# Performance work log

Measured on AMD Instinct MI355X. Metric: run time of the kernel, lower is better.

Reference implementation:

```python
import jax, jax.numpy as jnp
import numpy as np

N_ITERS = 2
N_NODES = 50000
N_EDGES = 400000
NODE_DIM = 128
EDGE_DIM = 128
MLP_HIDDEN = 128


def _gru_cell(x, h, W_ih, W_hh, b_ih, b_hh):
    # torch.nn.GRUCell math. W_ih: [3H, in], W_hh: [3H, H]
    gi = x @ W_ih.T + b_ih
    gh = h @ W_hh.T + b_hh
    i_r, i_z, i_n = jnp.split(gi, 3, axis=-1)
    h_r, h_z, h_n = jnp.split(gh, 3, axis=-1)
    r = jax.nn.sigmoid(i_r + h_r)
    z = jax.nn.sigmoid(i_z + h_z)
    n = jnp.tanh(i_n + r * h_n)
    return (1.0 - z) * n + z * h


def _edge_softmax(logits, dst, num_nodes):
    # logits: [E], normalized over incoming edges of each dst node
    m = jax.ops.segment_max(logits, dst, num_segments=num_nodes)
    e = jnp.exp(logits - m[dst])
    s = jax.ops.segment_sum(e, dst, num_segments=num_nodes)
    return e / s[dst]


def setup_inputs() -> dict:
    key = jax.random.key(0)
    ks = jax.random.split(key, 20)
    s = 0.05
    inp = {
        'nf': jax.random.normal(ks[0], (N_NODES, NODE_DIM), jnp.float32),
        'ef': jax.random.normal(ks[1], (N_EDGES, EDGE_DIM), jnp.float32),
        'src': jax.random.randint(ks[2], (N_EDGES,), 0, N_NODES, jnp.int32),
        'dst': jax.random.randint(ks[3], (N_EDGES,), 0, N_NODES, jnp.int32),
        # edge GRUCell: input 2*node_dim -> hidden edge_dim
        'eW_ih': s * jax.random.normal(ks[4], (3 * EDGE_DIM, 2 * NODE_DIM), jnp.float32),
        'eW_hh': s * jax.random.normal(ks[5], (3 * EDGE_DIM, EDGE_DIM), jnp.float32),
        'eb_ih': s * jax.random.normal(ks[6], (3 * EDGE_DIM,), jnp.float32),
        'eb_hh': s * jax.random.normal(ks[7], (3 * EDGE_DIM,), jnp.float32),
        # node GRUCell: input edge_dim -> hidden node_dim
        'nW_ih': s * jax.random.normal(ks[8], (3 * NODE_DIM, EDGE_DIM), jnp.float32),
        'nW_hh': s * jax.random.normal(ks[9], (3 * NODE_DIM, NODE_DIM), jnp.float32),
        'nb_ih': s * jax.random.normal(ks[10], (3 * NODE_DIM,), jnp.float32),
        'nb_hh': s * jax.random.normal(ks[11], (3 * NODE_DIM,), jnp.float32),
        # attention MLP: edge_dim -> hidden -> 1
        'aW1': s * jax.random.normal(ks[12], (EDGE_DIM, MLP_HIDDEN), jnp.float32),
        'ab1': jnp.zeros((MLP_HIDDEN,), jnp.float32),
        'aW2': s * jax.random.normal(ks[13], (MLP_HIDDEN, 1), jnp.float32),
        'ab2': jnp.zeros((1,), jnp.float32),
    }
    return inp


def reference(nf, ef, src, dst, eW_ih, eW_hh, eb_ih, eb_hh,
              nW_ih, nW_hh, nb_ih, nb_hh, aW1, ab1, aW2, ab2):
    num_nodes = nf.shape[0]
    for _ in range(N_ITERS):
        # per-edge GRU update: input = [src_h ; dst_h], hidden = edge feature
        x_e = jnp.concatenate([nf[src], nf[dst]], axis=-1)  # [E, 2*node_dim]
        uef = _gru_cell(x_e, ef, eW_ih, eW_hh, eb_ih, eb_hh)  # [E, edge_dim]
        # attention MLP + edge softmax over destination neighborhoods
        logits = (jax.nn.relu(uef @ aW1 + ab1) @ aW2 + ab2)[:, 0]  # [E]
        attn = _edge_softmax(logits, dst, num_nodes)  # [E]
        # weighted scatter-sum aggregation to destination nodes
        agg_m = jax.ops.segment_sum(uef * attn[:, None], dst, num_segments=num_nodes)
        # node GRU update
        unf = _gru_cell(agg_m, nf, nW_ih, nW_hh, nb_ih, nb_hh)  # [N, node_dim]
        nf, ef = unf, uef
    return (nf, ef)
```

## Files before the change

### kernel.cpp

```cpp
#include <hip/hip_runtime.h>

#define NN 50000
#define NE 400000
#define DIM 128

typedef __bf16 bf16x8 __attribute__((ext_vector_type(8)));
typedef float f32x4 __attribute__((ext_vector_type(4)));
typedef unsigned short u16;

#define MFMA16 __builtin_amdgcn_mfma_f32_16x16x32_bf16

__device__ __forceinline__ u16 f2b(float f){ __bf16 b=(__bf16)f; return __builtin_bit_cast(u16,b); }
__device__ __forceinline__ float b2f(u16 h){ unsigned u = ((unsigned)h)<<16; return __builtin_bit_cast(float,u); }
__device__ __forceinline__ float sigm(float x){ return 1.0f/(1.0f+__expf(-x)); }
__device__ __forceinline__ float tanh_(float x){ float e=__expf(2.0f*x); return 1.0f-2.0f/(e+1.0f); }
__device__ __forceinline__ bf16x8 ldb8(const u16* p){ return *reinterpret_cast<const bf16x8*>(p); }

#define GLOAD_LDS(gp, lp) __builtin_amdgcn_global_load_lds( \
    (const __attribute__((address_space(1))) void*)(gp),    \
    (__attribute__((address_space(3))) void*)(lp), 16, 0, 0)

__global__ void f2b_kernel(const float* __restrict__ in, u16* __restrict__ out, int n4){
  int i = blockIdx.x*blockDim.x + threadIdx.x;
  int st = gridDim.x*blockDim.x;
  for (; i<n4; i+=st){
    float4 v = reinterpret_cast<const float4*>(in)[i];
    ushort4 o = { f2b(v.x), f2b(v.y), f2b(v.z), f2b(v.w) };
    reinterpret_cast<ushort4*>(out)[i] = o;
  }
}

__global__ void transpose128_kernel(const float* __restrict__ in, u16* __restrict__ out){
  int i = blockIdx.x*blockDim.x + threadIdx.x;
  int k = i>>7, n = i&127;
  out[n*128+k] = f2b(in[i]);
}

__global__ void zero_kernel(int* p, int n){
  int i = blockIdx.x*blockDim.x + threadIdx.x; if (i<n) p[i]=0;
}
__global__ void hist_kernel(const int* __restrict__ dst, int* __restrict__ counts, int n){
  int i = blockIdx.x*blockDim.x + threadIdx.x; if (i<n) atomicAdd(&counts[dst[i]],1);
}
__global__ void scan_kernel(const int* __restrict__ counts, int* __restrict__ rowp,
                            int* __restrict__ cursor, int n){
  __shared__ int buf[1024];
  __shared__ int run;
  const int t = threadIdx.x;
  if (t==0) run = 0;
  __syncthreads();
  for (int base=0; base<n; base+=1024){
    int v = (base+t<n) ? counts[base+t] : 0;
    buf[t]=v; __syncthreads();
    for (int off=1; off<1024; off<<=1){
      int x = (t>=off) ? buf[t-off] : 0;
      __syncthreads();
      buf[t]+=x; __syncthreads();
    }
    int incl = buf[t];
    int br = run;
    __syncthreads();
    if (base+t<n){ int ex = br+incl-v; rowp[base+t]=ex; cursor[base+t]=ex; }
    if (t==1023) run = br+incl;
    __syncthreads();
  }
  if (t==0) rowp[n]=run;
}
__global__ void scatter_kernel(const int* __restrict__ dst, int* __restrict__ cursor,
                               int* __restrict__ eids, int n){
  int i = blockIdx.x*blockDim.x + threadIdx.x;
  if (i<n){ int p = atomicAdd(&cursor[dst[i]],1); eids[p]=i; }
}

__global__ __launch_bounds__(512, 4)
void edge_kernel(const int* __restrict__ src, const int* __restrict__ dst,
                 const u16* __restrict__ nfb, u16* __restrict__ efb,
                 const u16* __restrict__ Wih, const u16* __restrict__ Whh,
                 const float* __restrict__ bih, const float* __restrict__ bhh,
                 const u16* __restrict__ aW1T, const float* __restrict__ ab1,
                 const float* __restrict__ aW2, const float* __restrict__ ab2,
                 float* __restrict__ logits, float* __restrict__ ef32out)
{
  __shared__ __align__(16) u16 wbuf[2*36*512];
  const int wave = threadIdx.x>>6, lane = threadIdx.x&63;
  const int r16 = lane&15, kq = lane>>4;
  const long base = (long)blockIdx.x*128 + wave*16;
  const long e = base + r16;

  auto stage = [&](int c){
    u16* bufp = wbuf + (c&1)*36*512;
    if (c < 8){
      for (int f = wave; f < 36; f += 8){
        const u16* g;
        if (f < 24){ const int gt = f>>3, s = f&7;
          g = Wih + (long)(gt*128 + c*16 + r16)*256 + s*32 + kq*8; }
        else { const int q = f-24, gt = q>>2, s = q&3;
          g = Whh + (long)(gt*128 + c*16 + r16)*128 + s*32 + kq*8; }
        GLOAD_LDS(g, bufp + f*512);
      }
    } else if (c == 8){
      for (int f = wave; f < 32; f += 8){
        const int t = f>>2, s = f&3;
        GLOAD_LDS(aW1T + (long)(t*16 + r16)*128 + s*32 + kq*8, bufp + f*512);
      }
    }
  };

  const u16* sp = nfb + (long)src[e]*DIM;
  const u16* dp = nfb + (long)dst[e]*DIM;
  const u16* ep = efb + e*DIM;
  bf16x8 ag[8], ae[4];
#pragma unroll
  for (int s=0;s<4;++s){
    ag[s]   = ldb8(sp + s*32 + kq*8);
    ag[s+4] = ldb8(dp + s*32 + kq*8);
    ae[s]   = ldb8(ep + s*32 + kq*8);
  }
  stage(0);
  __syncthreads();

  const f32x4 vzero = {0.f,0.f,0.f,0.f};

#pragma unroll 1
  for (int c=0;c<8;++c){
    stage(c+1);
    const int oc = c*16 + r16;
    const float bir=bih[oc], biz=bih[DIM+oc], bin=bih[2*DIM+oc];
    const float bhr=bhh[oc], bhz=bhh[DIM+oc], bhn=bhh[2*DIM+oc];
    float h0p[4];
#pragma unroll
    for (int r=0;r<4;++r) h0p[r] = b2f(efb[(base+kq*4+r)*DIM + oc]);

    const u16* lb = wbuf + (c&1)*36*512 + lane*8;
    f32x4 ar=vzero, az=vzero, an=vzero, hr=vzero, hz=vzero, hn=vzero;
#pragma unroll
    for (int s=0;s<8;++s){
      ar = MFMA16(ag[s], ldb8(lb + ( s   )*512), ar,0,0,0);
      az = MFMA16(ag[s], ldb8(lb + ( 8+s )*512), az,0,0,0);
      an = MFMA16(ag[s], ldb8(lb + (16+s )*512), an,0,0,0);
    }
#pragma unroll
    for (int s=0;s<4;++s){
      hr = MFMA16(ae[s], ldb8(lb + (24+s)*512), hr,0,0,0);
      hz = MFMA16(ae[s], ldb8(lb + (28+s)*512), hz,0,0,0);
      hn = MFMA16(ae[s], ldb8(lb + (32+s)*512), hn,0,0,0);
    }
#pragma unroll
    for (int r=0;r<4;++r){
      const long er = base + kq*4 + r;
      float rg = sigm(ar[r]+bir + hr[r]+bhr);
      float zg = sigm(az[r]+biz + hz[r]+bhz);
      float ng = tanh_(an[r]+bin + rg*(hn[r]+bhn));
      float u  = (1.0f-zg)*ng + zg*h0p[r];
      efb[er*DIM+oc] = f2b(u);
      if (ef32out) ef32out[er*DIM+oc] = u;
    }
    __syncthreads();
  }

  bf16x8 ua[4];
#pragma unroll
  for (int s=0;s<4;++s) ua[s] = ldb8(ep + s*32 + kq*8);
  const u16* lb = wbuf + lane*8;
  float part[4] = {0.f,0.f,0.f,0.f};
#pragma unroll 1
  for (int t=0;t<8;++t){
    f32x4 h = vzero;
#pragma unroll
    for (int s=0;s<4;++s)
      h = MFMA16(ua[s], ldb8(lb + (t*4+s)*512), h,0,0,0);
    const int cc = t*16 + r16;
    const float b1 = ab1[cc], w2 = aW2[cc];
#pragma unroll
    for (int r=0;r<4;++r) part[r] += fmaxf(h[r]+b1, 0.f)*w2;
  }
#pragma unroll
  for (int off=1; off<16; off<<=1){
#pragma unroll
    for (int r=0;r<4;++r) part[r] += __shfl_xor(part[r], off, 64);
  }
  if (r16==0){
    const float b2v = ab2[0];
#pragma unroll
    for (int r=0;r<4;++r) logits[base + kq*4 + r] = part[r] + b2v;
  }
}

__global__ __launch_bounds__(256)
void agg_kernel(const int* __restrict__ rowp, const int* __restrict__ eids,
                const float* __restrict__ logits, const u16* __restrict__ uefb,
                u16* __restrict__ aggb)
{
  const int wave = threadIdx.x>>6, lane = threadIdx.x&63;
  const int v = blockIdx.x*4 + wave;
  if (v>=NN) return;
  const int p0 = rowp[v], deg = rowp[v+1]-p0;
  float ax=0.f, ay=0.f;
  if (deg>0){
    float mx = -__builtin_inff();
    for (int i=lane; i<deg; i+=64) mx = fmaxf(mx, logits[eids[p0+i]]);
#pragma unroll
    for (int off=32; off; off>>=1) mx = fmaxf(mx, __shfl_xor(mx, off, 64));
    float ss = 0.f;
    for (int i=lane; i<deg; i+=64) ss += __expf(logits[eids[p0+i]] - mx);
#pragma unroll
    for (int off=32; off; off>>=1) ss += __shfl_xor(ss, off, 64);
    const float inv = 1.0f/ss;
    int i = 0;
    for (; i+2<=deg; i+=2){
      const int e0 = eids[p0+i], e1 = eids[p0+i+1];
      const float l0 = logits[e0], l1 = logits[e1];
      const unsigned q0 = *reinterpret_cast<const unsigned*>(uefb + (long)e0*DIM + lane*2);
      const unsigned q1 = *reinterpret_cast<const unsigned*>(uefb + (long)e1*DIM + lane*2);
      const float a0 = __expf(l0-mx)*inv, a1 = __expf(l1-mx)*inv;
      ax += a0*b2f((u16)q0) + a1*b2f((u16)q1);
      ay += a0*b2f((u16)(q0>>16)) + a1*b2f((u16)(q1>>16));
    }
    if (i<deg){
      const int e0 = eids[p0+i];
      const float a0 = __expf(logits[e0]-mx)*inv;
      const unsigned q0 = *reinterpret_cast<const unsigned*>(uefb + (long)e0*DIM + lane*2);
      ax += a0*b2f((u16)q0);
      ay += a0*b2f((u16)(q0>>16));
    }
  }
  unsigned pack = (unsigned)f2b(ax) | ((unsigned)f2b(ay)<<16);
  *reinterpret_cast<unsigned*>(aggb + (long)v*DIM + lane*2) = pack;
}

__global__ __launch_bounds__(512, 4)
void node_kernel(const u16* __restrict__ aggb, u16* __restrict__ nfb,
                 const float* nf32, float* unf32,
                 const u16* __restrict__ Wih, const u16* __restrict__ Whh,
                 const float* __restrict__ bih, const float* __restrict__ bhh)
{
  __shared__ __align__(16) u16 wbuf[2*24*512];
  const int wave = threadIdx.x>>6, lane = threadIdx.x&63;
  const int r16 = lane&15, kq = lane>>4;
  const long tbase = (long)blockIdx.x*128 + wave*16;
  const long v = tbase + r16;
  const long vcl = (v < NN) ? v : (NN-1);

  auto stage = [&](int c){
    if (c >= 8) return;
    u16* bufp = wbuf + (c&1)*24*512;
    for (int f = wave; f < 24; f += 8){
      const u16* g;
      if (f < 12){ const int gt = f>>2, s = f&3;
        g = Wih + (long)(gt*128 + c*16 + r16)*128 + s*32 + kq*8; }
      else { const int q = f-12, gt = q>>2, s = q&3;
        g = Whh + (long)(gt*128 + c*16 + r16)*128 + s*32 + kq*8; }
      GLOAD_LDS(g, bufp + f*512);
    }
  };

  bf16x8 xa[4], ha[4];
#pragma unroll
  for (int s=0;s<4;++s){
    xa[s] = ldb8(aggb + vcl*DIM + s*32 + kq*8);
    ha[s] = ldb8(nfb  + vcl*DIM + s*32 + kq*8);
  }
  stage(0);
  __syncthreads();

  const f32x4 vzero = {0.f,0.f,0.f,0.f};

#pragma unroll 1
  for (int c=0;c<8;++c){
    stage(c+1);
    const int oc = c*16 + r16;
    const float bir=bih[oc], biz=bih[DIM+oc], bin=bih[2*DIM+oc];
    const float bhr=bhh[oc], bhz=bhh[DIM+oc], bhn=bhh[2*DIM+oc];
    float h0p[4];
#pragma unroll
    for (int r=0;r<4;++r){
      const long rr = tbase + kq*4 + r;
      h0p[r] = (rr < NN) ? nf32[rr*DIM+oc] : 0.f;
    }
    const u16* lb = wbuf + (c&1)*24*512 + lane*8;
    f32x4 ar=vzero, az=vzero, an=vzero, hr=vzero, hz=vzero, hn=vzero;
#pragma unroll
    for (int s=0;s<4;++s){
      ar=MFMA16(xa[s], ldb8(lb + ( s   )*512), ar,0,0,0);
      az=MFMA16(xa[s], ldb8(lb + ( 4+s)*512), az,0,0,0);
      an=MFMA16(xa[s], ldb8(lb + ( 8+s)*512), an,0,0,0);
      hr=MFMA16(ha[s], ldb8(lb + (12+s)*512), hr,0,0,0);
      hz=MFMA16(ha[s], ldb8(lb + (16+s)*512), hz,0,0,0);
      hn=MFMA16(ha[s], ldb8(lb + (20+s)*512), hn,0,0,0);
    }
#pragma unroll
    for (int r=0;r<4;++r){
      const long rr = tbase + kq*4 + r;
      if (rr < NN){
        float rg = sigm(ar[r]+bir + hr[r]+bhr);
        float zg = sigm(az[r]+biz + hz[r]+bhz);
        float ng = tanh_(an[r]+bin + rg*(hn[r]+bhn));
        float u  = (1.0f-zg)*ng + zg*h0p[r];
        unf32[rr*DIM+oc] = u;
        nfb[rr*DIM+oc] = f2b(u);
      }
    }
    __syncthreads();
  }
}

extern "C" void kernel_launch(void* const* d_in, const int* in_sizes, int n_in,
                              void* d_out, int out_size, void* d_ws, size_t ws_size,
                              hipStream_t stream)
{
  const float* nf_in = (const float*)d_in[0];
  const float* ef_in = (const float*)d_in[1];
  const int*   src   = (const int*)d_in[2];
  const int*   dst   = (const int*)d_in[3];
  const float* eWih  = (const float*)d_in[4];
  const float* eWhh  = (const float*)d_in[5];
  const float* ebih  = (const float*)d_in[6];
  const float* ebhh  = (const float*)d_in[7];
  const float* nWih  = (const float*)d_in[8];
  const float* nWhh  = (const float*)d_in[9];
  const float* nbih  = (const float*)d_in[10];
  const float* nbhh  = (const float*)d_in[11];
  const float* aW1   = (const float*)d_in[12];
  const float* ab1   = (const float*)d_in[13];
  const float* aW2   = (const float*)d_in[14];
  const float* ab2   = (const float*)d_in[15];

  float* nf_out = (float*)d_out;
  float* ef_out = nf_out + (size_t)NN*DIM;

  char* p = (char*)d_ws;
  auto carve = [&](size_t bytes)->void*{ void* r = (void*)p; p += (bytes + 255) & ~(size_t)255; return r; };
  u16* efb    = (u16*)carve((size_t)NE*DIM*2);
  u16* nfb    = (u16*)carve((size_t)NN*DIM*2);
  u16* aggb   = (u16*)carve((size_t)NN*DIM*2);
  float* logits = (float*)carve((size_t)NE*4);
  int* eids   = (int*)carve((size_t)NE*4);
  int* counts = (int*)carve((size_t)NN*4);
  int* rowp   = (int*)carve((size_t)(NN+1)*4);
  int* cursor = (int*)carve((size_t)NN*4);
  u16* bWih   = (u16*)carve((size_t)384*256*2);
  u16* bWhh   = (u16*)carve((size_t)384*128*2);
  u16* bnWih  = (u16*)carve((size_t)384*128*2);
  u16* bnWhh  = (u16*)carve((size_t)384*128*2);
  u16* baW1T  = (u16*)carve((size_t)128*128*2);

  f2b_kernel<<<2048,256,0,stream>>>(nf_in, nfb, NN*DIM/4);
  f2b_kernel<<<2048,256,0,stream>>>(ef_in, efb, NE*DIM/4);
  f2b_kernel<<<96,256,0,stream>>>(eWih, bWih, 384*256/4);
  f2b_kernel<<<48,256,0,stream>>>(eWhh, bWhh, 384*128/4);
  f2b_kernel<<<48,256,0,stream>>>(nWih, bnWih, 384*128/4);
  f2b_kernel<<<48,256,0,stream>>>(nWhh, bnWhh, 384*128/4);
  transpose128_kernel<<<64,256,0,stream>>>(aW1, baW1T);

  zero_kernel<<<(NN+255)/256,256,0,stream>>>(counts, NN);
  hist_kernel<<<(NE+255)/256,256,0,stream>>>(dst, counts, NE);
  scan_kernel<<<1,1024,0,stream>>>(counts, rowp, cursor, NN);
  scatter_kernel<<<(NE+255)/256,256,0,stream>>>(dst, cursor, eids, NE);

  for (int it=0; it<2; ++it){
    const float* nf_cur = (it==0) ? nf_in : nf_out;
    float* efout32 = (it==1) ? ef_out : nullptr;
    edge_kernel<<<NE/128,512,0,stream>>>(src, dst, nfb, efb,
                                         bWih, bWhh, ebih, ebhh,
                                         baW1T, ab1, aW2, ab2, logits, efout32);
    agg_kernel<<<(NN+3)/4,256,0,stream>>>(rowp, eids, logits, efb, aggb);
    node_kernel<<<(NN+127)/128,512,0,stream>>>(aggb, nfb, nf_cur, nf_out,
                                               bnWih, bnWhh, nbih, nbhh);
  }
}
```

Measured before the change: 928.9 us.

## Single-buffer edge kernel weight staging to raise occupancy

Replaces the double-buffered LDS weight staging in the edge GRU kernel with a single buffer. After the MFMAs of each chunk, a barrier is added and the next chunk's weights are staged so the load overlaps the gate math. Halving LDS use lets the launch bound rise from 4 to 6 blocks per SM, trading prefetch overlap with compute for more resident waves to hide gather latency. It also hoists base pointers for the bias, efb and ef32 accesses and groups the fp32 stores.

```diff
diff --git a/kernel.cpp b/kernel.cpp
--- a/kernel.cpp
+++ b/kernel.cpp
@@ -72,7 +72,7 @@
   if (i<n){ int p = atomicAdd(&cursor[dst[i]],1); eids[p]=i; }
 }
 
-__global__ __launch_bounds__(512, 4)
+__global__ __launch_bounds__(512, 6)
 void edge_kernel(const int* __restrict__ src, const int* __restrict__ dst,
                  const u16* __restrict__ nfb, u16* __restrict__ efb,
                  const u16* __restrict__ Wih, const u16* __restrict__ Whh,
@@ -81,14 +81,13 @@
                  const float* __restrict__ aW2, const float* __restrict__ ab2,
                  float* __restrict__ logits, float* __restrict__ ef32out)
 {
-  __shared__ __align__(16) u16 wbuf[2*36*512];
+  __shared__ __align__(16) u16 wbuf[36*512];
   const int wave = threadIdx.x>>6, lane = threadIdx.x&63;
   const int r16 = lane&15, kq = lane>>4;
   const long base = (long)blockIdx.x*128 + wave*16;
   const long e = base + r16;
 
   auto stage = [&](int c){
-    u16* bufp = wbuf + (c&1)*36*512;
     if (c < 8){
       for (int f = wave; f < 36; f += 8){
         const u16* g;
@@ -96,12 +95,12 @@
           g = Wih + (long)(gt*128 + c*16 + r16)*256 + s*32 + kq*8; }
         else { const int q = f-24, gt = q>>2, s = q&3;
           g = Whh + (long)(gt*128 + c*16 + r16)*128 + s*32 + kq*8; }
-        GLOAD_LDS(g, bufp + f*512);
+        GLOAD_LDS(g, wbuf + f*512);
       }
-    } else if (c == 8){
+    } else {
       for (int f = wave; f < 32; f += 8){
         const int t = f>>2, s = f&3;
-        GLOAD_LDS(aW1T + (long)(t*16 + r16)*128 + s*32 + kq*8, bufp + f*512);
+        GLOAD_LDS(aW1T + (long)(t*16 + r16)*128 + s*32 + kq*8, wbuf + f*512);
       }
     }
   };
@@ -119,41 +118,51 @@
   stage(0);
   __syncthreads();
 
+  u16*  ebase = efb + (base + kq*4)*DIM + r16;
+  float* fbase = ef32out ? ef32out + (base + kq*4)*DIM + r16 : nullptr;
+  const float* bi0 = bih + r16;
+  const float* bh0 = bhh + r16;
+
   const f32x4 vzero = {0.f,0.f,0.f,0.f};
+  const u16* lbase = wbuf + lane*8;
 
 #pragma unroll 1
   for (int c=0;c<8;++c){
+    const int c16 = c*16;
+    const float bir=bi0[c16], biz=bi0[c16+DIM], bin=bi0[c16+2*DIM];
+    const float bhr=bh0[c16], bhz=bh0[c16+DIM], bhn=bh0[c16+2*DIM];
+    float h0p[4];
+#pragma unroll
+    for (int r=0;r<4;++r) h0p[r] = b2f(ebase[r*DIM + c16]);
+
+    f32x4 ar=vzero, az=vzero, an=vzero, hr=vzero, hz=vzero, hn=vzero;
+#pragma unroll
+    for (int s=0;s<8;++s){
+      ar = MFMA16(ag[s], ldb8(lbase + ( s   )*512), ar,0,0,0);
+      az = MFMA16(ag[s], ldb8(lbase + ( 8+s )*512), az,0,0,0);
+      an = MFMA16(ag[s], ldb8(lbase + (16+s )*512), an,0,0,0);
+    }
+#pragma unroll
+    for (int s=0;s<4;++s){
+      hr = MFMA16(ae[s], ldb8(lbase + (24+s)*512), hr,0,0,0);
+      hz = MFMA16(ae[s], ldb8(lbase + (28+s)*512), hz,0,0,0);
+      hn = MFMA16(ae[s], ldb8(lbase + (32+s)*512), hn,0,0,0);
+    }
+    __syncthreads();
     stage(c+1);
-    const int oc = c*16 + r16;
-    const float bir=bih[oc], biz=bih[DIM+oc], bin=bih[2*DIM+oc];
-    const float bhr=bhh[oc], bhz=bhh[DIM+oc], bhn=bhh[2*DIM+oc];
-    float h0p[4];
-#pragma unroll
-    for (int r=0;r<4;++r) h0p[r] = b2f(efb[(base+kq*4+r)*DIM + oc]);
-
-    const u16* lb = wbuf + (c&1)*36*512 + lane*8;
-    f32x4 ar=vzero, az=vzero, an=vzero, hr=vzero, hz=vzero, hn=vzero;
-#pragma unroll
-    for (int s=0;s<8;++s){
-      ar = MFMA16(ag[s], ldb8(lb + ( s   )*512), ar,0,0,0);
-      az = MFMA16(ag[s], ldb8(lb + ( 8+s )*512), az,0,0,0);
-      an = MFMA16(ag[s], ldb8(lb + (16+s )*512), an,0,0,0);
-    }
-#pragma unroll
-    for (int s=0;s<4;++s){
-      hr = MFMA16(ae[s], ldb8(lb + (24+s)*512), hr,0,0,0);
-      hz = MFMA16(ae[s], ldb8(lb + (28+s)*512), hz,0,0,0);
-      hn = MFMA16(ae[s], ldb8(lb + (32+s)*512), hn,0,0,0);
-    }
+    float uv[4];
 #pragma unroll
     for (int r=0;r<4;++r){
-      const long er = base + kq*4 + r;
       float rg = sigm(ar[r]+bir + hr[r]+bhr);
       float zg = sigm(az[r]+biz + hz[r]+bhz);
       float ng = tanh_(an[r]+bin + rg*(hn[r]+bhn));
       float u  = (1.0f-zg)*ng + zg*h0p[r];
-      efb[er*DIM+oc] = f2b(u);
-      if (ef32out) ef32out[er*DIM+oc] = u;
+      ebase[r*DIM + c16] = f2b(u);
+      uv[r] = u;
+    }
+    if (fbase){
+#pragma unroll
+      for (int r=0;r<4;++r) fbase[r*DIM + c16] = uv[r];
     }
     __syncthreads();
   }
@@ -161,14 +170,13 @@
   bf16x8 ua[4];
 #pragma unroll
   for (int s=0;s<4;++s) ua[s] = ldb8(ep + s*32 + kq*8);
-  const u16* lb = wbuf + lane*8;
   float part[4] = {0.f,0.f,0.f,0.f};
 #pragma unroll 1
   for (int t=0;t<8;++t){
     f32x4 h = vzero;
 #pragma unroll
     for (int s=0;s<4;++s)
-      h = MFMA16(ua[s], ldb8(lb + (t*4+s)*512), h,0,0,0);
+      h = MFMA16(ua[s], ldb8(lbase + (t*4+s)*512), h,0,0,0);
     const int cc = t*16 + r16;
     const float b1 = ab1[cc], w2 = aW2[cc];
 #pragma unroll
```

Result: slower. 1.233 ms (+32.8%).
